# Optimization experiments

Measured on AMD Instinct MI355X. Metric: run time of the kernel, lower is better.

## Reference

```python
import jax, jax.numpy as jnp
import numpy as np

E, F, H = 8, 5632, 2048
T = 8192


def setup_inputs() -> dict:
    key = jax.random.key(0)
    k1, k2, k3, k4 = jax.random.split(key, 4)
    s_w = 1.0 / np.sqrt(H)
    return {
        "expert_idx": 3,
        "hidden_states": jax.random.normal(k1, (T, H), dtype=jnp.float32),
        "fc1_1": jax.random.normal(k2, (E, F, H), dtype=jnp.float32) * s_w,
        "fc1_2": jax.random.normal(k3, (E, F, H), dtype=jnp.float32) * s_w,
        "fc2": jax.random.normal(k4, (E, H, F), dtype=jnp.float32) * (1.0 / np.sqrt(F)),
    }


def reference(expert_idx, hidden_states, fc1_1, fc1_2, fc2):
    # Select this expert's weights: [F,H], [F,H], [H,F]
    w1 = fc1_1[expert_idx]
    w2 = fc1_2[expert_idx]
    w3 = fc2[expert_idx]
    # SwiGLU FFN: silu(x @ w1^T) * (x @ w2^T) @ w3^T
    gate = jnp.einsum("th,fh->tf", hidden_states, w1)
    up = jnp.einsum("th,fh->tf", hidden_states, w2)
    fc1_out = jax.nn.silu(gate) * up  # [T, F]
    out = jnp.einsum("tf,hf->th", fc1_out, w3)  # [T, H]
    return out
```

## Files before the change

kernel.cpp:

```cpp
#include <hip/hip_runtime.h>
#include <hip/hip_bf16.h>

#define T_DIM 8192
#define H_DIM 2048
#define F_DIM 5632

typedef __attribute__((ext_vector_type(4))) float f32x4;
typedef __attribute__((ext_vector_type(8))) short bf16x8;

static __device__ __forceinline__ void gload16(const void* g, void* l) {
    __builtin_amdgcn_global_load_lds(
        (const __attribute__((address_space(1))) void*)g,
        (__attribute__((address_space(3))) void*)l,
        16, 0, 0);
}

static __device__ __forceinline__ unsigned short f2bf(float f) {
    unsigned int u = __float_as_uint(f);
    u += 0x7fffu + ((u >> 16) & 1u);
    return (unsigned short)(u >> 16);
}

__global__ __launch_bounds__(256)
void cvt_x(const float* __restrict__ src, unsigned short* __restrict__ dst, long n)
{
    const long stride = (long)gridDim.x * blockDim.x;
    for (long i = (long)blockIdx.x * blockDim.x + threadIdx.x; i * 4 < n; i += stride) {
        const float4 v = *(const float4*)(src + i * 4);
        ushort4 o;
        o.x = f2bf(v.x); o.y = f2bf(v.y); o.z = f2bf(v.z); o.w = f2bf(v.w);
        *(ushort4*)(dst + i * 4) = o;
    }
}

__global__ __launch_bounds__(256)
void cvt_w(const float* __restrict__ w1, const float* __restrict__ w2,
           const float* __restrict__ w3, const int* __restrict__ eidx,
           unsigned short* __restrict__ W1b, unsigned short* __restrict__ W2b,
           unsigned short* __restrict__ W3b)
{
    const long seg = (long)F_DIM * H_DIM;
    const long e   = (long)(*eidx);
    const long nchunks = 3 * seg / 4;
    const long stride = (long)gridDim.x * blockDim.x;
    for (long i = (long)blockIdx.x * blockDim.x + threadIdx.x; i < nchunks; i += stride) {
        const long t = i * 4;
        const int  s = (int)(t / seg);
        const long o = t - (long)s * seg;
        const float* src = (s == 0 ? w1 : s == 1 ? w2 : w3) + e * seg + o;
        unsigned short* dst = (s == 0 ? W1b : s == 1 ? W2b : W3b) + o;
        const float4 v = *(const float4*)src;
        ushort4 ov;
        ov.x = f2bf(v.x); ov.y = f2bf(v.y); ov.z = f2bf(v.z); ov.w = f2bf(v.w);
        *(ushort4*)dst = ov;
    }
}

static __device__ __forceinline__ void stage_half(const unsigned short* __restrict__ g,
                                                  long grow0, long ldk, long kb,
                                                  unsigned short* l, int t, int i0)
{
    const int r  = t >> 3;
    const int cc = ((t & 7) ^ (r & 7)) << 3;
    #pragma unroll
    for (int i = i0; i < i0 + 2; ++i)
        gload16(g + (grow0 + i * 64 + r) * ldk + kb + cc,
                l + i * 4096 + t * 8);
}

static __device__ __forceinline__ void stage_fc1B(const unsigned short* __restrict__ W1,
                                                  const unsigned short* __restrict__ W2,
                                                  long bn128, long kb,
                                                  unsigned short* l, int t, int i0)
{
    const int r  = t >> 3;
    const int cc = ((t & 7) ^ (r & 7)) << 3;
    #pragma unroll
    for (int i = i0; i < i0 + 2; ++i) {
        const int br = i * 64 + r;
        const int g2 = br >> 6;
        const int rr = br & 63;
        const unsigned short* src = (rr < 32) ? W1 : W2;
        const long row = bn128 + g2 * 32 + (rr & 31);
        gload16(src + row * H_DIM + kb + cc, l + i * 4096 + t * 8);
    }
}

static __device__ __forceinline__ bf16x8 ldsfrag(const unsigned short* base,
                                                 int row, int kk, int q)
{
    return *(const bf16x8*)(base + row * 64 + (((kk * 4 + q) ^ (row & 7)) << 3));
}

#define PHASE_BODY(p, STAGE_STMT)                                              \
    {                                                                          \
        bf16x8 af[2][2];                                                       \
        _Pragma("unroll")                                                      \
        for (int l_ = 0; l_ < 2; ++l_)                                         \
            _Pragma("unroll")                                                  \
            for (int kk = 0; kk < 2; ++kk)                                     \
                af[l_][kk] = ldsfrag(la, wm * 128 + (p) * 32 + l_ * 16 + lr, kk, q); \
        STAGE_STMT;                                                            \
        __builtin_amdgcn_s_barrier();                                          \
        __builtin_amdgcn_s_setprio(1);                                         \
        _Pragma("unroll")                                                      \
        for (int l_ = 0; l_ < 2; ++l_)                                         \
            _Pragma("unroll")                                                  \
            for (int ni = 0; ni < 4; ++ni)                                     \
                _Pragma("unroll")                                              \
                for (int kk = 0; kk < 2; ++kk)                                 \
                    acc[(p) * 2 + l_][ni] = __builtin_amdgcn_mfma_f32_16x16x32_bf16( \
                        af[l_][kk], bf[ni][kk], acc[(p) * 2 + l_][ni], 0, 0, 0);     \
        __builtin_amdgcn_s_setprio(0);                                         \
        __builtin_amdgcn_s_barrier();                                          \
    }

struct FD { long arow, bn128, kb; };
static __device__ __forceinline__ FD fdec(int f, int t0, int x)
{
    const int vt = t0 + (f >> 5);
    FD d;
    d.bn128 = (long)(vt >> 2) * 128;
    d.arow  = (long)(x * 4 + (vt & 3)) * 256;
    d.kb    = (long)(f & 31) * 64;
    return d;
}

__global__ __launch_bounds__(512, 2)
void gemm_fc1(const unsigned short* __restrict__ X,
              const unsigned short* __restrict__ W1,
              const unsigned short* __restrict__ W2,
              unsigned short* __restrict__ Hout)
{
    __shared__ __align__(16) unsigned short sAll[4 * 16384];

    const int tid  = threadIdx.x;
    const int lane = tid & 63;
    const int wid  = tid >> 6;
    const int wm   = wid >> 2;
    const int wn   = wid & 3;
    const int q    = lane >> 4;
    const int lr   = lane & 15;

    const int bid = blockIdx.x;
    const int x   = bid & 7;
    const int y   = bid >> 3;
    const int ntt = (y < 16) ? 6 : 5;
    const int t0  = (y < 16) ? 6 * y : 5 * y + 16;
    const int FTOT = ntt * 32;

    f32x4 acc[8][4] = {};

    {
        FD d0 = fdec(0, t0, x);
        stage_half(X, d0.arow, H_DIM, d0.kb, sAll, tid, 0);
        stage_half(X, d0.arow, H_DIM, d0.kb, sAll, tid, 2);
        stage_fc1B(W1, W2, d0.bn128, d0.kb, sAll + 16384, tid, 0);
        stage_fc1B(W1, W2, d0.bn128, d0.kb, sAll + 16384, tid, 2);
        FD d1 = fdec(1, t0, x);
        stage_fc1B(W1, W2, d1.bn128, d1.kb, sAll + 49152, tid, 0);
        stage_fc1B(W1, W2, d1.bn128, d1.kb, sAll + 49152, tid, 2);
    }

    for (int f = 0; f < FTOT; ++f) {
        unsigned short* la = sAll + (f & 1) * 32768;
        unsigned short* lb = la + 16384;

        if (f + 1 < FTOT) {
            FD dn = fdec(f + 1, t0, x);
            unsigned short* na = sAll + ((f + 1) & 1) * 32768;
            stage_half(X, dn.arow, H_DIM, dn.kb, na, tid, 0);
            stage_half(X, dn.arow, H_DIM, dn.kb, na, tid, 2);
            asm volatile("s_waitcnt vmcnt(8)" ::: "memory");
        } else {
            asm volatile("s_waitcnt vmcnt(0)" ::: "memory");
        }
        __builtin_amdgcn_s_barrier();

        bf16x8 bf[4][2];
        #pragma unroll
        for (int ni = 0; ni < 4; ++ni)
            #pragma unroll
            for (int kk = 0; kk < 2; ++kk)
                bf[ni][kk] = ldsfrag(lb, wn * 64 + ni * 16 + lr, kk, q);

        PHASE_BODY(0, {})
        PHASE_BODY(1, { if (f + 2 < FTOT) { FD d2 = fdec(f + 2, t0, x);
                                            stage_fc1B(W1, W2, d2.bn128, d2.kb, lb, tid, 0); } })
        PHASE_BODY(2, { if (f + 2 < FTOT) { FD d2 = fdec(f + 2, t0, x);
                                            stage_fc1B(W1, W2, d2.bn128, d2.kb, lb, tid, 2); } })
        PHASE_BODY(3, {})

        if ((f & 31) == 31) {
            const int vt = t0 + (f >> 5);
            const int bn = vt >> 2;
            const int bm = x * 4 + (vt & 3);
            const long orow = (long)bm * 256 + wm * 128;
            const long ocol = (long)bn * 128 + wn * 32;
            #pragma unroll
            for (int mi = 0; mi < 8; ++mi) {
                #pragma unroll
                for (int nj = 0; nj < 2; ++nj)
                    #pragma unroll
                    for (int r = 0; r < 4; ++r) {
                        const float g = acc[mi][nj][r];
                        const float u = acc[mi][nj + 2][r];
                        const float h = __fdividef(g, 1.0f + __expf(-g)) * u;
                        Hout[(orow + mi * 16 + q * 4 + r) * (long)F_DIM +
                             (ocol + nj * 16 + lr)] = f2bf(h);
                    }
                #pragma unroll
                for (int ni = 0; ni < 4; ++ni)
                    acc[mi][ni] = (f32x4){0.f, 0.f, 0.f, 0.f};
            }
        }
    }
}

__global__ __launch_bounds__(512, 2)
void gemm_out(const unsigned short* __restrict__ A,
              const unsigned short* __restrict__ B,
              float* __restrict__ Out)
{
    constexpr int NK  = F_DIM / 64;
    constexpr int NBN = H_DIM / 256;

    __shared__ __align__(16) unsigned short sAll[4 * 16384];

    const int tid  = threadIdx.x;
    const int lane = tid & 63;
    const int wid  = tid >> 6;
    const int wm   = wid >> 2;
    const int wn   = wid & 3;
    const int q    = lane >> 4;
    const int lr   = lane & 15;

    const int nwg = gridDim.x;
    const int bid = blockIdx.x;
    const int cpx = nwg >> 3;
    const int swz = (bid & 7) * cpx + (bid >> 3);
    const int bm  = swz / NBN;
    const int bn  = swz % NBN;

    const long arow0 = (long)bm * 256;
    const long brow0 = (long)bn * 256;

    f32x4 acc[8][4] = {};

    stage_half(A, arow0, F_DIM, 0,  sAll,          tid, 0);
    stage_half(A, arow0, F_DIM, 0,  sAll,          tid, 2);
    stage_half(B, brow0, F_DIM, 0,  sAll + 16384,  tid, 0);
    stage_half(B, brow0, F_DIM, 0,  sAll + 16384,  tid, 2);
    stage_half(B, brow0, F_DIM, 64, sAll + 49152,  tid, 0);
    stage_half(B, brow0, F_DIM, 64, sAll + 49152,  tid, 2);

    for (int j = 0; j < NK; ++j) {
        unsigned short* la = sAll + (j & 1) * 32768;
        unsigned short* lb = la + 16384;

        if (j + 1 < NK) {
            unsigned short* na = sAll + ((j + 1) & 1) * 32768;
            stage_half(A, arow0, F_DIM, (long)(j + 1) * 64, na, tid, 0);
            stage_half(A, arow0, F_DIM, (long)(j + 1) * 64, na, tid, 2);
            asm volatile("s_waitcnt vmcnt(8)" ::: "memory");
        } else {
            asm volatile("s_waitcnt vmcnt(0)" ::: "memory");
        }
        __builtin_amdgcn_s_barrier();

        bf16x8 bf[4][2];
        #pragma unroll
        for (int ni = 0; ni < 4; ++ni)
            #pragma unroll
            for (int kk = 0; kk < 2; ++kk)
                bf[ni][kk] = ldsfrag(lb, wn * 64 + ni * 16 + lr, kk, q);

        PHASE_BODY(0, {})
        PHASE_BODY(1, { if (j + 2 < NK) stage_half(B, brow0, F_DIM, (long)(j + 2) * 64, lb, tid, 0); })
        PHASE_BODY(2, { if (j + 2 < NK) stage_half(B, brow0, F_DIM, (long)(j + 2) * 64, lb, tid, 2); })
        PHASE_BODY(3, {})
    }

    const long orow = (long)bm * 256 + wm * 128;
    const long ocol = (long)bn * 256 + wn * 64;
    #pragma unroll
    for (int mi = 0; mi < 8; ++mi)
        #pragma unroll
        for (int ni = 0; ni < 4; ++ni)
            #pragma unroll
            for (int r = 0; r < 4; ++r)
                Out[(orow + mi * 16 + q * 4 + r) * (long)H_DIM + (ocol + ni * 16 + lr)]
                    = acc[mi][ni][r];
}

extern "C" void kernel_launch(void* const* d_in, const int* in_sizes, int n_in,
                              void* d_out, int out_size, void* d_ws, size_t ws_size,
                              hipStream_t stream)
{
    const int*   eidx = (const int*)d_in[0];
    const float* x    = (const float*)d_in[1];
    const float* w1   = (const float*)d_in[2];
    const float* w2   = (const float*)d_in[3];
    const float* w3   = (const float*)d_in[4];
    float* out = (float*)d_out;

    const size_t SZ_X = (size_t)T_DIM * H_DIM;
    const size_t SZ_W = (size_t)F_DIM * H_DIM;

    unsigned short* Xb  = (unsigned short*)d_ws;
    unsigned short* W1b = Xb  + SZ_X;
    unsigned short* W2b = W1b + SZ_W;
    unsigned short* W3b = W2b + SZ_W;
    unsigned short* Hb  = W3b + SZ_W;

    cvt_x<<<2048, 256, 0, stream>>>(x, Xb, (long)SZ_X);
    cvt_w<<<2048, 256, 0, stream>>>(w1, w2, w3, eidx, W1b, W2b, W3b);

    gemm_fc1<<<256, 512, 0, stream>>>(Xb, W1b, W2b, Hb);
    gemm_out<<<256, 512, 0, stream>>>(Hb, W3b, out);
}
```

Measured before the change: 582.7 us.

## Pre-interleave gate/up weights and replace persistent fc1 loop with one-tile-per-block grid

The weight conversion now writes W1 and W2 interleaved into a single matrix in 32-row groups per 128-row tile, so the fc1 GEMM can stage B with the plain stage_half loader. The persistent fc1 kernel, which walked several output tiles per block with balanced 6/5 tile counts, becomes one 256x128 tile per block over a 32x44 grid (1408 blocks). This drops per-iteration tile decoding and the mid-loop epilogue branch, at the cost of persistence and with a possible wave-quantization tail. The gemm_out grid is written as an expression that still evaluates to 256.

```diff
diff --git a/kernel.cpp b/kernel.cpp
--- a/kernel.cpp
+++ b/kernel.cpp
@@ -36,8 +36,7 @@
 __global__ __launch_bounds__(256)
 void cvt_w(const float* __restrict__ w1, const float* __restrict__ w2,
            const float* __restrict__ w3, const int* __restrict__ eidx,
-           unsigned short* __restrict__ W1b, unsigned short* __restrict__ W2b,
-           unsigned short* __restrict__ W3b)
+           unsigned short* __restrict__ W12, unsigned short* __restrict__ W3b)
 {
     const long seg = (long)F_DIM * H_DIM;
     const long e   = (long)(*eidx);
@@ -47,12 +46,19 @@
         const long t = i * 4;
         const int  s = (int)(t / seg);
         const long o = t - (long)s * seg;
-        const float* src = (s == 0 ? w1 : s == 1 ? w2 : w3) + e * seg + o;
-        unsigned short* dst = (s == 0 ? W1b : s == 1 ? W2b : W3b) + o;
-        const float4 v = *(const float4*)src;
+        const float4 v = *(const float4*)((s == 0 ? w1 : s == 1 ? w2 : w3) + e * seg + o);
         ushort4 ov;
         ov.x = f2bf(v.x); ov.y = f2bf(v.y); ov.z = f2bf(v.z); ov.w = f2bf(v.w);
-        *(ushort4*)dst = ov;
+        if (s == 2) {
+            *(ushort4*)(W3b + o) = ov;
+        } else {
+            const long r   = o >> 11;
+            const long col = o & 2047;
+            const int  l7  = (int)(r & 127);
+            const long R   = (r >> 7) * 256 + (l7 >> 5) * 64 + (l7 & 31)
+                           + (s == 1 ? 32 : 0);
+            *(ushort4*)(W12 + R * 2048 + col) = ov;
+        }
     }
 }
 
@@ -66,24 +72,6 @@
     for (int i = i0; i < i0 + 2; ++i)
         gload16(g + (grow0 + i * 64 + r) * ldk + kb + cc,
                 l + i * 4096 + t * 8);
-}
-
-static __device__ __forceinline__ void stage_fc1B(const unsigned short* __restrict__ W1,
-                                                  const unsigned short* __restrict__ W2,
-                                                  long bn128, long kb,
-                                                  unsigned short* l, int t, int i0)
-{
-    const int r  = t >> 3;
-    const int cc = ((t & 7) ^ (r & 7)) << 3;
-    #pragma unroll
-    for (int i = i0; i < i0 + 2; ++i) {
-        const int br = i * 64 + r;
-        const int g2 = br >> 6;
-        const int rr = br & 63;
-        const unsigned short* src = (rr < 32) ? W1 : W2;
-        const long row = bn128 + g2 * 32 + (rr & 31);
-        gload16(src + row * H_DIM + kb + cc, l + i * 4096 + t * 8);
-    }
 }
 
 static __device__ __forceinline__ bf16x8 ldsfrag(const unsigned short* base,
@@ -115,23 +103,13 @@
         __builtin_amdgcn_s_barrier();                                          \
     }
 
-struct FD { long arow, bn128, kb; };
-static __device__ __forceinline__ FD fdec(int f, int t0, int x)
-{
-    const int vt = t0 + (f >> 5);
-    FD d;
-    d.bn128 = (long)(vt >> 2) * 128;
-    d.arow  = (long)(x * 4 + (vt & 3)) * 256;
-    d.kb    = (long)(f & 31) * 64;
-    return d;
-}
-
 __global__ __launch_bounds__(512, 2)
 void gemm_fc1(const unsigned short* __restrict__ X,
-              const unsigned short* __restrict__ W1,
-              const unsigned short* __restrict__ W2,
+              const unsigned short* __restrict__ W12,
               unsigned short* __restrict__ Hout)
 {
+    constexpr int NK = H_DIM / 64;
+
     __shared__ __align__(16) unsigned short sAll[4 * 16384];
 
     const int tid  = threadIdx.x;
@@ -144,33 +122,30 @@
 
     const int bid = blockIdx.x;
     const int x   = bid & 7;
-    const int y   = bid >> 3;
-    const int ntt = (y < 16) ? 6 : 5;
-    const int t0  = (y < 16) ? 6 * y : 5 * y + 16;
-    const int FTOT = ntt * 32;
+    const int i   = bid >> 3;
+    const int bn  = i >> 2;
+    const int bm  = x * 4 + (i & 3);
+
+    const long arow0 = (long)bm * 256;
+    const long brow0 = (long)bn * 256;
 
     f32x4 acc[8][4] = {};
 
-    {
-        FD d0 = fdec(0, t0, x);
-        stage_half(X, d0.arow, H_DIM, d0.kb, sAll, tid, 0);
-        stage_half(X, d0.arow, H_DIM, d0.kb, sAll, tid, 2);
-        stage_fc1B(W1, W2, d0.bn128, d0.kb, sAll + 16384, tid, 0);
-        stage_fc1B(W1, W2, d0.bn128, d0.kb, sAll + 16384, tid, 2);
-        FD d1 = fdec(1, t0, x);
-        stage_fc1B(W1, W2, d1.bn128, d1.kb, sAll + 49152, tid, 0);
-        stage_fc1B(W1, W2, d1.bn128, d1.kb, sAll + 49152, tid, 2);
-    }
-
-    for (int f = 0; f < FTOT; ++f) {
-        unsigned short* la = sAll + (f & 1) * 32768;
+    stage_half(X,   arow0, H_DIM, 0,  sAll,          tid, 0);
+    stage_half(X,   arow0, H_DIM, 0,  sAll,          tid, 2);
+    stage_half(W12, brow0, H_DIM, 0,  sAll + 16384,  tid, 0);
+    stage_half(W12, brow0, H_DIM, 0,  sAll + 16384,  tid, 2);
+    stage_half(W12, brow0, H_DIM, 64, sAll + 49152,  tid, 0);
+    stage_half(W12, brow0, H_DIM, 64, sAll + 49152,  tid, 2);
+
+    for (int j = 0; j < NK; ++j) {
+        unsigned short* la = sAll + (j & 1) * 32768;
         unsigned short* lb = la + 16384;
 
-        if (f + 1 < FTOT) {
-            FD dn = fdec(f + 1, t0, x);
-            unsigned short* na = sAll + ((f + 1) & 1) * 32768;
-            stage_half(X, dn.arow, H_DIM, dn.kb, na, tid, 0);
-            stage_half(X, dn.arow, H_DIM, dn.kb, na, tid, 2);
+        if (j + 1 < NK) {
+            unsigned short* na = sAll + ((j + 1) & 1) * 32768;
+            stage_half(X, arow0, H_DIM, (long)(j + 1) * 64, na, tid, 0);
+            stage_half(X, arow0, H_DIM, (long)(j + 1) * 64, na, tid, 2);
             asm volatile("s_waitcnt vmcnt(8)" ::: "memory");
         } else {
             asm volatile("s_waitcnt vmcnt(0)" ::: "memory");
@@ -185,36 +160,25 @@
                 bf[ni][kk] = ldsfrag(lb, wn * 64 + ni * 16 + lr, kk, q);
 
         PHASE_BODY(0, {})
-        PHASE_BODY(1, { if (f + 2 < FTOT) { FD d2 = fdec(f + 2, t0, x);
-                                            stage_fc1B(W1, W2, d2.bn128, d2.kb, lb, tid, 0); } })
-        PHASE_BODY(2, { if (f + 2 < FTOT) { FD d2 = fdec(f + 2, t0, x);
-                                            stage_fc1B(W1, W2, d2.bn128, d2.kb, lb, tid, 2); } })
+        PHASE_BODY(1, { if (j + 2 < NK) stage_half(W12, brow0, H_DIM, (long)(j + 2) * 64, lb, tid, 0); })
+        PHASE_BODY(2, { if (j + 2 < NK) stage_half(W12, brow0, H_DIM, (long)(j + 2) * 64, lb, tid, 2); })
         PHASE_BODY(3, {})
-
-        if ((f & 31) == 31) {
-            const int vt = t0 + (f >> 5);
-            const int bn = vt >> 2;
-            const int bm = x * 4 + (vt & 3);
-            const long orow = (long)bm * 256 + wm * 128;
-            const long ocol = (long)bn * 128 + wn * 32;
-            #pragma unroll
-            for (int mi = 0; mi < 8; ++mi) {
-                #pragma unroll
-                for (int nj = 0; nj < 2; ++nj)
-                    #pragma unroll
-                    for (int r = 0; r < 4; ++r) {
-                        const float g = acc[mi][nj][r];
-                        const float u = acc[mi][nj + 2][r];
-                        const float h = __fdividef(g, 1.0f + __expf(-g)) * u;
-                        Hout[(orow + mi * 16 + q * 4 + r) * (long)F_DIM +
-                             (ocol + nj * 16 + lr)] = f2bf(h);
-                    }
-                #pragma unroll
-                for (int ni = 0; ni < 4; ++ni)
-                    acc[mi][ni] = (f32x4){0.f, 0.f, 0.f, 0.f};
+    }
+
+    const long orow = (long)bm * 256 + wm * 128;
+    const long ocol = (long)bn * 128 + wn * 32;
+    #pragma unroll
+    for (int mi = 0; mi < 8; ++mi)
+        #pragma unroll
+        for (int nj = 0; nj < 2; ++nj)
+            #pragma unroll
+            for (int r = 0; r < 4; ++r) {
+                const float g = acc[mi][nj][r];
+                const float u = acc[mi][nj + 2][r];
+                const float h = __fdividef(g, 1.0f + __expf(-g)) * u;
+                Hout[(orow + mi * 16 + q * 4 + r) * (long)F_DIM +
+                     (ocol + nj * 16 + lr)] = f2bf(h);
             }
-        }
-    }
 }
 
 __global__ __launch_bounds__(512, 2)
@@ -308,14 +272,13 @@
     const size_t SZ_W = (size_t)F_DIM * H_DIM;
 
     unsigned short* Xb  = (unsigned short*)d_ws;
-    unsigned short* W1b = Xb  + SZ_X;
-    unsigned short* W2b = W1b + SZ_W;
-    unsigned short* W3b = W2b + SZ_W;
+    unsigned short* W12 = Xb  + SZ_X;
+    unsigned short* W3b = W12 + 2 * SZ_W;
     unsigned short* Hb  = W3b + SZ_W;
 
     cvt_x<<<2048, 256, 0, stream>>>(x, Xb, (long)SZ_X);
-    cvt_w<<<2048, 256, 0, stream>>>(w1, w2, w3, eidx, W1b, W2b, W3b);
-
-    gemm_fc1<<<256, 512, 0, stream>>>(Xb, W1b, W2b, Hb);
-    gemm_out<<<256, 512, 0, stream>>>(Hb, W3b, out);
-}
+    cvt_w<<<2048, 256, 0, stream>>>(w1, w2, w3, eidx, W12, W3b);
+
+    gemm_fc1<<<(T_DIM / 256) * (F_DIM / 128), 512, 0, stream>>>(Xb, W12, Hb);
+    gemm_out<<<(T_DIM / 256) * (H_DIM / 256), 512, 0, stream>>>(Hb, W3b, out);
+}
```

Measured after the change: 551.8 us. -5.3%, faster.
